# Kernel optimization log

Measured on AMD Instinct MI355X. Metric: run time of the kernel, lower is better.

The kernel has to match this reference:

```python
import jax, jax.numpy as jnp
import numpy as np
import math

L, B, T, S, D, H = 6, 4, 1024, 1024, 1024, 16
HD = D // H
SCALE = 1.0 / math.sqrt(HD)
EPS = 1e-5


def _ln(x, w, b):
    m = x.mean(-1, keepdims=True)
    v = ((x - m) ** 2).mean(-1, keepdims=True)
    return (x - m) * jax.lax.rsqrt(v + EPS) * w + b


def _mha(xq, xkv, qw, qb, kw, kb, vw, vb, ow, ob, mask):
    b, t, _ = xq.shape
    s = xkv.shape[1]
    q = (xq @ qw.T + qb).reshape(b, t, H, HD).transpose(0, 2, 1, 3)
    k = (xkv @ kw.T + kb).reshape(b, s, H, HD).transpose(0, 2, 1, 3)
    v = (xkv @ vw.T + vb).reshape(b, s, H, HD).transpose(0, 2, 1, 3)
    scores = jnp.einsum('bhqd,bhkd->bhqk', q, k) * SCALE
    scores = jnp.where(mask == 0, -jnp.inf, scores)
    attn = jax.nn.softmax(scores, axis=-1)  # dropout is identity (eval)
    o = jnp.einsum('bhqk,bhkd->bhqd', attn, v).transpose(0, 2, 1, 3).reshape(b, t, D)
    return o @ ow.T + ob


def _ffn(x, f1w, f1b, f2w, f2b, fnw, fnb):
    h = jax.nn.gelu(x @ f1w.T + f1b, approximate=False)
    y = h @ f2w.T + f2b
    return x + _ln(y, fnw, fnb)


def setup_inputs() -> dict:
    key = jax.random.key(0)
    ks = jax.random.split(key, 16)
    wf = lambda k: jax.random.normal(k, (L, D, D), jnp.float32) * 0.02
    zb = jnp.zeros((L, D), jnp.float32)
    ones = jnp.ones((L, D), jnp.float32)
    inp = {
        'x': jax.random.normal(ks[0], (B, T, D), jnp.float32),
        'enc_outputs': jax.random.normal(ks[1], (B, S, D), jnp.float32),
        'sqw': wf(ks[2]), 'sqb': zb, 'skw': wf(ks[3]), 'skb': zb,
        'svw': wf(ks[4]), 'svb': zb, 'sow': wf(ks[5]), 'sob': zb,
        'cqw': wf(ks[6]), 'cqb': zb, 'ckw': wf(ks[7]), 'ckb': zb,
        'cvw': wf(ks[8]), 'cvb': zb, 'cow': wf(ks[9]), 'cob': zb,
        'f1w': wf(ks[10]), 'f1b': zb, 'f2w': wf(ks[11]), 'f2b': zb,
        'fnw': ones, 'fnb': zb,
        'l1w': ones, 'l1b': zb, 'l2w': ones, 'l2b': zb, 'l3w': ones, 'l3b': zb,
        'src_mask': jnp.ones((1, 1, T, S), jnp.int32),
        'tgt_mask': jnp.tril(jnp.ones((T, T), jnp.int32))[None, None],
    }
    return inp


def reference(x, enc_outputs, sqw, sqb, skw, skb, svw, svb, sow, sob,
              cqw, cqb, ckw, ckb, cvw, cvb, cow, cob,
              f1w, f1b, f2w, f2b, fnw, fnb,
              l1w, l1b, l2w, l2b, l3w, l3b, src_mask, tgt_mask):
    for l in range(L):
        sa = _mha(x, x, sqw[l], sqb[l], skw[l], skb[l], svw[l], svb[l], sow[l], sob[l], tgt_mask)
        x = _ln(x + sa, l1w[l], l1b[l])
        ca = _mha(x, enc_outputs, cqw[l], cqb[l], ckw[l], ckb[l], cvw[l], cvb[l], cow[l], cob[l], src_mask)
        x = _ln(x + ca, l2w[l], l2b[l])
        ff = _ffn(x, f1w[l], f1b[l], f2w[l], f2b[l], fnw[l], fnb[l])
        x = _ln(x + ff, l3w[l], l3b[l])
    return x
```

## Files before the change

### kernel.cpp

```cpp
#include <hip/hip_runtime.h>
#include <stdint.h>

typedef unsigned short u16;
typedef unsigned int u32;
typedef __bf16 bf16x8 __attribute__((ext_vector_type(8)));
typedef float f32x4 __attribute__((ext_vector_type(4)));
typedef u16 u16x8 __attribute__((ext_vector_type(8)));
typedef u16 u16x4 __attribute__((ext_vector_type(4)));
typedef u32 u32x2 __attribute__((ext_vector_type(2)));

#define MFMA16(A, B, C) __builtin_amdgcn_mfma_f32_16x16x32_bf16((A), (B), (C), 0, 0, 0)

#define GLOAD_LDS16(GP, LP)                                                    \
  __builtin_amdgcn_global_load_lds(                                            \
      (__attribute__((address_space(1))) void*)(GP),                           \
      (__attribute__((address_space(3))) void*)(LP), 16, 0, 0)

__device__ __forceinline__ u16 f2bf(float f) {
  return __builtin_bit_cast(u16, (__bf16)f);
}

__device__ __forceinline__ float bf2f(u16 v) {
  return __builtin_bit_cast(float, ((u32)v) << 16);
}

__device__ __forceinline__ float exp2_raw(float x) {
  float r;
  asm("v_exp_f32 %0, %1\n\ts_nop 0" : "=v"(r) : "v"(x));
  return r;
}

__device__ __forceinline__ u32 cvt_pk_bf16(float lo, float hi) {
  u32 r;
  asm("v_cvt_pk_bf16_f32 %0, %1, %2" : "=v"(r) : "v"(lo), "v"(hi));
  return r;
}

#define SC2 0.1803368801111204f

struct WPtrs {
  const float* p[10];
};

__global__ __launch_bounds__(256) void wcvt_kernel(WPtrs w, u16* __restrict__ dst, int loff) {
  const int mat = blockIdx.y;
  const int i = blockIdx.x * 256 + threadIdx.x;
  float4 v = ((const float4*)(w.p[mat] + loff))[i];
  u16x4 o = {f2bf(v.x), f2bf(v.y), f2bf(v.z), f2bf(v.w)};
  ((u16x4*)dst)[(size_t)mat * gridDim.x * 256 + i] = o;
}

struct GemmArgs {
  const u16* A[3];
  const u16* W[3];
  const float* bias[3];
  u16* C[3];
  float scale[3];
};

__global__ __launch_bounds__(256, 4) void gemm_bt(GemmArgs g) {
  const int mat = blockIdx.y >> 3;
  const int n0 = (blockIdx.y & 7) * 128;
  const int m0 = blockIdx.x * 128;
  const int kz = blockIdx.z;
  const int kn = 16 / gridDim.z;
  const u16* __restrict__ A = g.A[mat];
  const u16* __restrict__ W = g.W[mat];

  __shared__ u16 As[128][64];
  __shared__ u16 Bs[128][64];

  const int tid = threadIdx.x;
  const int lane = tid & 63;
  const int wv = tid >> 6;
  const int wm = (wv >> 1) * 64;
  const int wn = (wv & 1) * 64;
  const int fr = lane & 15;
  const int fg = lane >> 4;

  f32x4 acc[4][4];
#pragma unroll
  for (int i = 0; i < 4; ++i)
#pragma unroll
    for (int j = 0; j < 4; ++j)
#pragma unroll
      for (int r = 0; r < 4; ++r) acc[i][j][r] = 0.f;

  const int row8 = lane >> 3;
  const int csw = ((lane & 7) ^ row8) * 8;
  const u16* ga = A + (size_t)(m0 + wv * 32 + row8) * 1024 + csw + kz * kn * 64;
  const u16* gb = W + (size_t)(n0 + wv * 32 + row8) * 1024 + csw + kz * kn * 64;

  for (int kt = 0; kt < kn; ++kt) {
    __syncthreads();
#pragma unroll
    for (int i = 0; i < 4; ++i) {
      GLOAD_LDS16(ga + (size_t)i * 8 * 1024, &As[wv * 32 + i * 8][0]);
      GLOAD_LDS16(gb + (size_t)i * 8 * 1024, &Bs[wv * 32 + i * 8][0]);
    }
    ga += 64;
    gb += 64;
    __syncthreads();
#pragma unroll
    for (int ks = 0; ks < 2; ++ks) {
      bf16x8 af[4], bfr[4];
#pragma unroll
      for (int i = 0; i < 4; ++i) {
        af[i] = *(const bf16x8*)&As[wm + i * 16 + fr][((ks * 4 + fg) ^ (fr & 7)) * 8];
        bfr[i] = *(const bf16x8*)&Bs[wn + i * 16 + fr][((ks * 4 + fg) ^ (fr & 7)) * 8];
      }
#pragma unroll
      for (int mi = 0; mi < 4; ++mi)
#pragma unroll
        for (int ni = 0; ni < 4; ++ni) acc[mi][ni] = MFMA16(af[mi], bfr[ni], acc[mi][ni]);
    }
  }

  const float* __restrict__ bias = g.bias[mat];
  const float scl = g.scale[mat];
  float bv[4];
#pragma unroll
  for (int ni = 0; ni < 4; ++ni) bv[ni] = (kz == 0) ? bias[n0 + wn + ni * 16 + fr] : 0.f;

  u16* __restrict__ C = g.C[mat] + (size_t)kz * (4096 * 1024);
#pragma unroll
  for (int mi = 0; mi < 4; ++mi) {
#pragma unroll
    for (int ni = 0; ni < 4; ++ni) {
      const int col = n0 + wn + ni * 16 + fr;
#pragma unroll
      for (int r = 0; r < 4; ++r) {
        const int row = m0 + wm + mi * 16 + fg * 4 + r;
        C[(size_t)row * 1024 + col] = f2bf((acc[mi][ni][r] + bv[ni]) * scl);
      }
    }
  }
}

template <int EPI>
__global__ __launch_bounds__(256, 4) void gemm_bt64(GemmArgs g) {
  const int n0 = blockIdx.y * 128;
  const int m0 = blockIdx.x * 64;
  const int kz = blockIdx.z;
  const int kn = 16 / gridDim.z;
  const u16* __restrict__ A = g.A[0];
  const u16* __restrict__ W = g.W[0];

  __shared__ u16 As[64][64];
  __shared__ u16 Bs[128][64];

  const int tid = threadIdx.x;
  const int lane = tid & 63;
  const int wv = tid >> 6;
  const int wm = (wv >> 1) * 32;
  const int wn = (wv & 1) * 64;
  const int fr = lane & 15;
  const int fg = lane >> 4;

  f32x4 acc[2][4];
#pragma unroll
  for (int i = 0; i < 2; ++i)
#pragma unroll
    for (int j = 0; j < 4; ++j)
#pragma unroll
      for (int r = 0; r < 4; ++r) acc[i][j][r] = 0.f;

  const int row8 = lane >> 3;
  const int csw = ((lane & 7) ^ row8) * 8;
  const u16* ga = A + (size_t)(m0 + wv * 16 + row8) * 1024 + csw + kz * kn * 64;
  const u16* gb = W + (size_t)(n0 + wv * 32 + row8) * 1024 + csw + kz * kn * 64;

  for (int kt = 0; kt < kn; ++kt) {
    __syncthreads();
    GLOAD_LDS16(ga, &As[wv * 16][0]);
    GLOAD_LDS16(ga + (size_t)8 * 1024, &As[wv * 16 + 8][0]);
#pragma unroll
    for (int i = 0; i < 4; ++i)
      GLOAD_LDS16(gb + (size_t)i * 8 * 1024, &Bs[wv * 32 + i * 8][0]);
    ga += 64;
    gb += 64;
    __syncthreads();
#pragma unroll
    for (int ks = 0; ks < 2; ++ks) {
      bf16x8 af[2], bfr[4];
#pragma unroll
      for (int i = 0; i < 2; ++i)
        af[i] = *(const bf16x8*)&As[wm + i * 16 + fr][((ks * 4 + fg) ^ (fr & 7)) * 8];
#pragma unroll
      for (int i = 0; i < 4; ++i)
        bfr[i] = *(const bf16x8*)&Bs[wn + i * 16 + fr][((ks * 4 + fg) ^ (fr & 7)) * 8];
#pragma unroll
      for (int mi = 0; mi < 2; ++mi)
#pragma unroll
        for (int ni = 0; ni < 4; ++ni) acc[mi][ni] = MFMA16(af[mi], bfr[ni], acc[mi][ni]);
    }
  }

  const float* __restrict__ bias = g.bias[0];
  float bv[4];
#pragma unroll
  for (int ni = 0; ni < 4; ++ni) bv[ni] = (kz == 0) ? bias[n0 + wn + ni * 16 + fr] : 0.f;

  u16* __restrict__ C = g.C[0] + (size_t)kz * (4096 * 1024);
#pragma unroll
  for (int mi = 0; mi < 2; ++mi) {
#pragma unroll
    for (int ni = 0; ni < 4; ++ni) {
      const int col = n0 + wn + ni * 16 + fr;
#pragma unroll
      for (int r = 0; r < 4; ++r) {
        const int row = m0 + wm + mi * 16 + fg * 4 + r;
        float v = acc[mi][ni][r] + bv[ni];
        if (EPI == 1) v = 0.5f * v * (1.0f + erff(v * 0.70710678118654752f));
        C[(size_t)row * 1024 + col] = f2bf(v);
      }
    }
  }
}

__global__ __launch_bounds__(512, 4) void attn_fwd(const u16* __restrict__ Q,
                                                   const u16* __restrict__ K,
                                                   const u16* __restrict__ V,
                                                   u16* __restrict__ O, int causal) {
  const int b = blockIdx.x >> 4;
  const int h = blockIdx.x & 15;
  const int qb = causal ? (7 - blockIdx.y) : blockIdx.y;
  const int tid = threadIdx.x;
  const int lane = tid & 63;
  const int wv = tid >> 6;
  const int fr = lane & 15;
  const int fg = lane >> 4;

  __shared__ u16 Ks[2][64][64];
  __shared__ u16 Vt[2][64][64];
  __shared__ u16 Plds[8][16][64];

  const int qrow0 = b * 1024 + qb * 128 + wv * 16;
  const int col0 = h * 64;

  const u16* qp = Q + (size_t)(qrow0 + fr) * 1024 + col0 + fg * 8;
  bf16x8 aQ0 = *(const bf16x8*)qp;
  bf16x8 aQ1 = *(const bf16x8*)(qp + 32);

  f32x4 ov[4];
#pragma unroll
  for (int i = 0; i < 4; ++i)
#pragma unroll
    for (int r = 0; r < 4; ++r) ov[i][r] = 0.f;
  float l_part = 0.f;

  const int kv_base = b * 1024;
  const int qg = qb * 128 + wv * 16 + fr;
  const int qg_max = qb * 128 + wv * 16 + 15;
  const int nt = causal ? (2 * qb + 2) : 16;

  const u16* gk0 = K + (size_t)(kv_base + wv * 16 + (lane >> 3)) * 1024 + col0 +
                   (((lane & 7) ^ (lane >> 3)) * 8);
  const int vt = tid - 256;
  const int kkp = vt & 31;
  const int d0 = (vt >> 5) * 8;
  const u16* gv0 = V + (size_t)(kv_base + 2 * kkp) * 1024 + col0 + d0;

#define STAGE_K(T, BUF)                                                        \
  if (wv < 4) {                                                                \
    const u16* gk = gk0 + (size_t)(T)*64 * 1024;                               \
    GLOAD_LDS16(gk, &Ks[BUF][wv * 16][0]);                                     \
    GLOAD_LDS16(gk + 8 * 1024, &Ks[BUF][wv * 16 + 8][0]);                      \
  }
#define LOAD_V(T)                                                              \
  if (tid >= 256) {                                                            \
    const u16* gvp = gv0 + (size_t)(T)*64 * 1024;                              \
    vr0 = *(const u16x8*)gvp;                                                  \
    vr1 = *(const u16x8*)(gvp + 1024);                                         \
  }
#define WRITE_V(BUF)                                                           \
  if (tid >= 256) {                                                            \
    _Pragma("unroll") for (int j = 0; j < 8; ++j) {                            \
      u32 pk = (u32)vr0[j] | ((u32)vr1[j] << 16);                              \
      *(u32*)&Vt[BUF][d0 + j][(((kkp >> 2) ^ j) * 8) + (kkp & 3) * 2] = pk;    \
    }                                                                          \
  }

  u16x8 vr0, vr1;
  STAGE_K(0, 0);
  LOAD_V(0);
  WRITE_V(0);

  for (int t = 0; t < nt; ++t) {
    const int cur = t & 1;
    __syncthreads();
    const bool pf = (t + 1 < nt);
    if (pf) {
      STAGE_K(t + 1, cur ^ 1);
      LOAD_V(t + 1);
    }

    const bool active = !causal || (t * 64 <= qg_max);
    if (active) {
      f32x4 st[4];
      __builtin_amdgcn_s_setprio(1);
#pragma unroll
      for (int hh = 0; hh < 4; ++hh) {
#pragma unroll
        for (int r = 0; r < 4; ++r) st[hh][r] = 0.f;
        const u16* krow = &Ks[cur][hh * 16 + fr][0];
        bf16x8 k0 = *(const bf16x8*)(krow + ((fg ^ (fr & 7)) * 8));
        bf16x8 k1 = *(const bf16x8*)(krow + (((4 + fg) ^ (fr & 7)) * 8));
        st[hh] = MFMA16(k0, aQ0, st[hh]);
        st[hh] = MFMA16(k1, aQ1, st[hh]);
      }
      __builtin_amdgcn_s_setprio(0);

      if (causal && t >= 2 * qb) {
#pragma unroll
        for (int hh = 0; hh < 4; ++hh)
#pragma unroll
          for (int r = 0; r < 4; ++r) {
            const int kkg = t * 64 + hh * 16 + fg * 4 + r;
            if (kkg > qg) st[hh][r] = -1e30f;
          }
      }

      float p[16];
#pragma unroll
      for (int hh = 0; hh < 4; ++hh)
#pragma unroll
        for (int r = 0; r < 4; ++r) {
          const float e = exp2_raw(st[hh][r]);
          p[hh * 4 + r] = e;
          l_part += e;
        }

#pragma unroll
      for (int hh = 0; hh < 4; ++hh) {
        u32x2 wpair = {cvt_pk_bf16(p[hh * 4 + 0], p[hh * 4 + 1]),
                       cvt_pk_bf16(p[hh * 4 + 2], p[hh * 4 + 3])};
        const int c = hh * 2 + (fg >> 1);
        *(u32x2*)&Plds[wv][fr][((c ^ (fr & 7)) * 8) + (fg & 1) * 4] = wpair;
      }
      bf16x8 pa[2];
#pragma unroll
      for (int ks = 0; ks < 2; ++ks)
        pa[ks] = *(const bf16x8*)&Plds[wv][fr][(((ks * 4 + fg) ^ (fr & 7)) * 8)];
      __builtin_amdgcn_s_setprio(1);
#pragma unroll
      for (int dt = 0; dt < 4; ++dt) {
#pragma unroll
        for (int ks = 0; ks < 2; ++ks) {
          bf16x8 bvv =
              *(const bf16x8*)&Vt[cur][dt * 16 + fr][(((ks * 4 + fg) ^ (fr & 7)) * 8)];
          ov[dt] = MFMA16(pa[ks], bvv, ov[dt]);
        }
      }
      __builtin_amdgcn_s_setprio(0);
    }

    if (pf) WRITE_V(cur ^ 1);
  }

  float ps = l_part;
  ps += __shfl_xor(ps, 16);
  ps += __shfl_xor(ps, 32);
  const float linv = 1.0f / ps;
  float fin[4];
#pragma unroll
  for (int r = 0; r < 4; ++r) fin[r] = __shfl(linv, fg * 4 + r);
#pragma unroll
  for (int dt = 0; dt < 4; ++dt)
#pragma unroll
    for (int r = 0; r < 4; ++r) {
      const int row = qrow0 + fg * 4 + r;
      const int col = col0 + dt * 16 + fr;
      O[(size_t)row * 1024 + col] = f2bf(ov[dt][r] * fin[r]);
    }
#undef STAGE_K
#undef LOAD_V
#undef WRITE_V
}

__device__ __forceinline__ float4 ld_bf4(const u16* p, size_t idx4) {
  u16x4 t = ((const u16x4*)p)[idx4];
  return make_float4(bf2f(t[0]), bf2f(t[1]), bf2f(t[2]), bf2f(t[3]));
}

__global__ __launch_bounds__(256) void ln_res_kernel(const u16* __restrict__ Xb_in,
                                                     const u16* __restrict__ T0,
                                                     const u16* __restrict__ T1, int nT,
                                                     const float* __restrict__ w,
                                                     const float* __restrict__ bia,
                                                     u16* __restrict__ Xb_out) {
  __shared__ float red[2][4];
  const int row = blockIdx.x;
  const int tid = threadIdx.x;
  const int lane = tid & 63, wv = tid >> 6;
  const size_t base4 = (size_t)row * 256;
  float4 xv = ld_bf4(Xb_in, base4 + tid);
  float4 tv = ld_bf4(T0, base4 + tid);
  float z0 = xv.x + tv.x, z1 = xv.y + tv.y, z2 = xv.z + tv.z, z3 = xv.w + tv.w;
  if (nT == 2) {
    float4 t1 = ld_bf4(T1, base4 + tid);
    z0 += t1.x; z1 += t1.y; z2 += t1.z; z3 += t1.w;
  }
  float s = z0 + z1 + z2 + z3;
  float ss = z0 * z0 + z1 * z1 + z2 * z2 + z3 * z3;
#pragma unroll
  for (int m = 1; m <= 32; m <<= 1) {
    s += __shfl_xor(s, m);
    ss += __shfl_xor(ss, m);
  }
  if (lane == 0) {
    red[0][wv] = s;
    red[1][wv] = ss;
  }
  __syncthreads();
  s = red[0][0] + red[0][1] + red[0][2] + red[0][3];
  ss = red[1][0] + red[1][1] + red[1][2] + red[1][3];
  const float mean = s * (1.f / 1024.f);
  const float var = ss * (1.f / 1024.f) - mean * mean;
  const float rs = rsqrtf(fmaxf(var, 0.f) + 1e-5f);
  float4 wv4 = ((const float4*)w)[tid];
  float4 bv4 = ((const float4*)bia)[tid];
  float o0 = (z0 - mean) * rs * wv4.x + bv4.x;
  float o1 = (z1 - mean) * rs * wv4.y + bv4.y;
  float o2 = (z2 - mean) * rs * wv4.z + bv4.z;
  float o3 = (z3 - mean) * rs * wv4.w + bv4.w;
  u16x4 ob = {f2bf(o0), f2bf(o1), f2bf(o2), f2bf(o3)};
  ((u16x4*)Xb_out)[base4 + tid] = ob;
}

__global__ __launch_bounds__(256) void ffn_ln_kernel(
    const u16* __restrict__ Xb, const u16* __restrict__ Y0, const u16* __restrict__ Y1,
    int nT, const float* __restrict__ fw_, const float* __restrict__ fb_,
    const float* __restrict__ w3, const float* __restrict__ b3, u16* __restrict__ Xb_out,
    float* __restrict__ Fout) {
  __shared__ float red[2][4];
  const int row = blockIdx.x;
  const int tid = threadIdx.x;
  const int lane = tid & 63, wv = tid >> 6;
  const size_t base4 = (size_t)row * 256;
  float4 yv = ld_bf4(Y0, base4 + tid);
  if (nT == 2) {
    float4 y1 = ld_bf4(Y1, base4 + tid);
    yv.x += y1.x; yv.y += y1.y; yv.z += y1.z; yv.w += y1.w;
  }
  float s = yv.x + yv.y + yv.z + yv.w;
  float ss = yv.x * yv.x + yv.y * yv.y + yv.z * yv.z + yv.w * yv.w;
#pragma unroll
  for (int m = 1; m <= 32; m <<= 1) {
    s += __shfl_xor(s, m);
    ss += __shfl_xor(ss, m);
  }
  if (lane == 0) {
    red[0][wv] = s;
    red[1][wv] = ss;
  }
  __syncthreads();
  s = red[0][0] + red[0][1] + red[0][2] + red[0][3];
  ss = red[1][0] + red[1][1] + red[1][2] + red[1][3];
  const float mean = s * (1.f / 1024.f);
  const float var = ss * (1.f / 1024.f) - mean * mean;
  const float rs = rsqrtf(fmaxf(var, 0.f) + 1e-5f);
  float4 xv = ld_bf4(Xb, base4 + tid);
  float4 fw4 = ((const float4*)fw_)[tid];
  float4 fb4 = ((const float4*)fb_)[tid];
  float z0 = 2.f * xv.x + (yv.x - mean) * rs * fw4.x + fb4.x;
  float z1 = 2.f * xv.y + (yv.y - mean) * rs * fw4.y + fb4.y;
  float z2 = 2.f * xv.z + (yv.z - mean) * rs * fw4.z + fb4.z;
  float z3 = 2.f * xv.w + (yv.w - mean) * rs * fw4.w + fb4.w;
  float s2 = z0 + z1 + z2 + z3;
  float ss2 = z0 * z0 + z1 * z1 + z2 * z2 + z3 * z3;
#pragma unroll
  for (int m = 1; m <= 32; m <<= 1) {
    s2 += __shfl_xor(s2, m);
    ss2 += __shfl_xor(ss2, m);
  }
  __syncthreads();
  if (lane == 0) {
    red[0][wv] = s2;
    red[1][wv] = ss2;
  }
  __syncthreads();
  s2 = red[0][0] + red[0][1] + red[0][2] + red[0][3];
  ss2 = red[1][0] + red[1][1] + red[1][2] + red[1][3];
  const float mean2 = s2 * (1.f / 1024.f);
  const float var2 = ss2 * (1.f / 1024.f) - mean2 * mean2;
  const float rs2 = rsqrtf(fmaxf(var2, 0.f) + 1e-5f);
  float4 w4 = ((const float4*)w3)[tid];
  float4 b4 = ((const float4*)b3)[tid];
  float o0 = (z0 - mean2) * rs2 * w4.x + b4.x;
  float o1 = (z1 - mean2) * rs2 * w4.y + b4.y;
  float o2 = (z2 - mean2) * rs2 * w4.z + b4.z;
  float o3 = (z3 - mean2) * rs2 * w4.w + b4.w;
  u16x4 ob = {f2bf(o0), f2bf(o1), f2bf(o2), f2bf(o3)};
  ((u16x4*)Xb_out)[base4 + tid] = ob;
  if (Fout) ((float4*)Fout)[base4 + tid] = make_float4(o0, o1, o2, o3);
}

__global__ __launch_bounds__(256) void cast2_kernel(const float* __restrict__ inA,
                                                    const float* __restrict__ inB,
                                                    u16* __restrict__ outA,
                                                    u16* __restrict__ outB) {
  const int bx = blockIdx.x;
  const float* in = (bx < 4096) ? inA : inB;
  u16* out = (bx < 4096) ? outA : outB;
  const size_t i = (size_t)(bx & 4095) * 256 + threadIdx.x;
  float4 v = ((const float4*)in)[i];
  u16x4 o = {f2bf(v.x), f2bf(v.y), f2bf(v.z), f2bf(v.w)};
  ((u16x4*)out)[i] = o;
}

extern "C" void kernel_launch(void* const* d_in, const int* in_sizes, int n_in, void* d_out,
                              int out_size, void* d_ws, size_t ws_size, hipStream_t stream) {
  const float* x_in = (const float*)d_in[0];
  const float* enc = (const float*)d_in[1];
  const float* sqw = (const float*)d_in[2];
  const float* sqb = (const float*)d_in[3];
  const float* skw = (const float*)d_in[4];
  const float* skb = (const float*)d_in[5];
  const float* svw = (const float*)d_in[6];
  const float* svb = (const float*)d_in[7];
  const float* sow = (const float*)d_in[8];
  const float* sob = (const float*)d_in[9];
  const float* cqw = (const float*)d_in[10];
  const float* cqb = (const float*)d_in[11];
  const float* ckw = (const float*)d_in[12];
  const float* ckb = (const float*)d_in[13];
  const float* cvw = (const float*)d_in[14];
  const float* cvb = (const float*)d_in[15];
  const float* cow = (const float*)d_in[16];
  const float* cob = (const float*)d_in[17];
  const float* f1w = (const float*)d_in[18];
  const float* f1b = (const float*)d_in[19];
  const float* f2w = (const float*)d_in[20];
  const float* f2b = (const float*)d_in[21];
  const float* fnw = (const float*)d_in[22];
  const float* fnb = (const float*)d_in[23];
  const float* l1w = (const float*)d_in[24];
  const float* l1b = (const float*)d_in[25];
  const float* l2w = (const float*)d_in[26];
  const float* l2b = (const float*)d_in[27];
  const float* l3w = (const float*)d_in[28];
  const float* l3b = (const float*)d_in[29];

  const size_t MB = 1024 * 1024;
  const int ALLW = (ws_size >= 200 * MB) ? 1 : 0;
  const int NS = (ws_size >= 90 * MB) ? 2 : 1;
  char* ws = (char*)d_ws;
  u16* tmpb = (u16*)ws;
  char* p = ws + (size_t)NS * 8 * MB;
  u16* xb = (u16*)p;   p += 8 * MB;
  u16* encb = (u16*)p; p += 8 * MB;
  u16* qbuf = (u16*)p; p += 8 * MB;
  u16* kbuf = (u16*)p; p += 8 * MB;
  u16* vbuf = (u16*)p; p += 8 * MB;
  u16* wbf = (u16*)p;
  u16* tmpb1 = tmpb + (size_t)4 * 1024 * 1024;
  const size_t W1M = 1024 * 1024;

  cast2_kernel<<<8192, 256, 0, stream>>>(x_in, enc, xb, encb);

  WPtrs wp;
  wp.p[0] = sqw; wp.p[1] = skw; wp.p[2] = svw; wp.p[3] = sow;
  wp.p[4] = cqw; wp.p[5] = ckw; wp.p[6] = cvw; wp.p[7] = cow;
  wp.p[8] = f1w; wp.p[9] = f2w;

  if (ALLW) wcvt_kernel<<<dim3(6144, 10), 256, 0, stream>>>(wp, wbf, 0);

  for (int l = 0; l < 6; ++l) {
    const size_t bo = (size_t)l * 1024;
    if (!ALLW) wcvt_kernel<<<dim3(1024, 10), 256, 0, stream>>>(wp, wbf, l * (int)W1M);
    #define WT(t) (ALLW ? (wbf + ((size_t)(t)*6 + l) * W1M) : (wbf + (size_t)(t)*W1M))

    GemmArgs g;
    g.scale[0] = SC2; g.scale[1] = 1.f; g.scale[2] = 1.f;
    g.A[0] = xb; g.A[1] = xb; g.A[2] = xb;
    g.W[0] = WT(0); g.W[1] = WT(1); g.W[2] = WT(2);
    g.bias[0] = sqb + bo; g.bias[1] = skb + bo; g.bias[2] = svb + bo;
    g.C[0] = qbuf; g.C[1] = kbuf; g.C[2] = vbuf;
    gemm_bt<<<dim3(32, 24, 1), 256, 0, stream>>>(g);
    attn_fwd<<<dim3(64, 8), 512, 0, stream>>>(qbuf, kbuf, vbuf, qbuf, 1);
    g.scale[0] = 1.f;
    g.A[0] = qbuf; g.W[0] = WT(3); g.bias[0] = sob + bo; g.C[0] = tmpb;
    gemm_bt64<0><<<dim3(64, 8, NS), 256, 0, stream>>>(g);
    ln_res_kernel<<<4096, 256, 0, stream>>>(xb, tmpb, tmpb1, NS, l1w + bo, l1b + bo, xb);

    g.scale[0] = SC2;
    g.A[0] = xb; g.A[1] = encb; g.A[2] = encb;
    g.W[0] = WT(4); g.W[1] = WT(5); g.W[2] = WT(6);
    g.bias[0] = cqb + bo; g.bias[1] = ckb + bo; g.bias[2] = cvb + bo;
    g.C[0] = qbuf; g.C[1] = kbuf; g.C[2] = vbuf;
    gemm_bt<<<dim3(32, 24, 1), 256, 0, stream>>>(g);
    attn_fwd<<<dim3(64, 8), 512, 0, stream>>>(qbuf, kbuf, vbuf, qbuf, 0);
    g.scale[0] = 1.f;
    g.A[0] = qbuf; g.W[0] = WT(7); g.bias[0] = cob + bo; g.C[0] = tmpb;
    gemm_bt64<0><<<dim3(64, 8, NS), 256, 0, stream>>>(g);
    ln_res_kernel<<<4096, 256, 0, stream>>>(xb, tmpb, tmpb1, NS, l2w + bo, l2b + bo, xb);

    g.A[0] = xb; g.W[0] = WT(8); g.bias[0] = f1b + bo; g.C[0] = kbuf;
    gemm_bt64<1><<<dim3(64, 8, 1), 256, 0, stream>>>(g);
    g.A[0] = kbuf; g.W[0] = WT(9); g.bias[0] = f2b + bo; g.C[0] = tmpb;
    gemm_bt64<0><<<dim3(64, 8, NS), 256, 0, stream>>>(g);
    float* fo = (l == 5) ? (float*)d_out : nullptr;
    ffn_ln_kernel<<<4096, 256, 0, stream>>>(xb, tmpb, tmpb1, NS, fnw + bo, fnb + bo, l3w + bo,
                                            l3b + bo, xb, fo);
    #undef WT
  }
}
```

Before: 1.311 ms.

## Split attention KV range across two blocks and merge partial outputs

Attention gains a template variant that splits each (batch, head, query-block) KV loop into two halves, indexed by blockIdx.z. Each half writes an unnormalised bf16 partial output plus per-row softmax denominators, and a new merge kernel sums the two partials and normalises. The aim is to double the number of attention blocks for better CU occupancy and to even out the load imbalance of causal blocks. In exchange it adds an extra kernel launch and extra memory traffic per attention call. The split path is only enabled when the workspace is large, and the all-weights threshold moves slightly to make room for the denominator buffer.

```diff
diff --git a/kernel.cpp b/kernel.cpp
--- a/kernel.cpp
+++ b/kernel.cpp
@@ -218,10 +218,12 @@
   }
 }
 
+template <int SPLIT>
 __global__ __launch_bounds__(512, 4) void attn_fwd(const u16* __restrict__ Q,
                                                    const u16* __restrict__ K,
                                                    const u16* __restrict__ V,
-                                                   u16* __restrict__ O, int causal) {
+                                                   u16* __restrict__ O,
+                                                   float* __restrict__ lb, int causal) {
   const int b = blockIdx.x >> 4;
   const int h = blockIdx.x & 15;
   const int qb = causal ? (7 - blockIdx.y) : blockIdx.y;
@@ -253,6 +255,12 @@
   const int qg = qb * 128 + wv * 16 + fr;
   const int qg_max = qb * 128 + wv * 16 + 15;
   const int nt = causal ? (2 * qb + 2) : 16;
+  int tbeg = 0, tend = nt;
+  if (SPLIT) {
+    const int h0 = nt >> 1;
+    tbeg = blockIdx.z ? h0 : 0;
+    tend = blockIdx.z ? nt : h0;
+  }
 
   const u16* gk0 = K + (size_t)(kv_base + wv * 16 + (lane >> 3)) * 1024 + col0 +
                    (((lane & 7) ^ (lane >> 3)) * 8);
@@ -282,14 +290,14 @@
   }
 
   u16x8 vr0, vr1;
-  STAGE_K(0, 0);
-  LOAD_V(0);
+  STAGE_K(tbeg, 0);
+  LOAD_V(tbeg);
   WRITE_V(0);
 
-  for (int t = 0; t < nt; ++t) {
-    const int cur = t & 1;
+  for (int t = tbeg; t < tend; ++t) {
+    const int cur = (t - tbeg) & 1;
     __syncthreads();
-    const bool pf = (t + 1 < nt);
+    const bool pf = (t + 1 < tend);
     if (pf) {
       STAGE_K(t + 1, cur ^ 1);
       LOAD_V(t + 1);
@@ -361,18 +369,34 @@
   float ps = l_part;
   ps += __shfl_xor(ps, 16);
   ps += __shfl_xor(ps, 32);
-  const float linv = 1.0f / ps;
-  float fin[4];
-#pragma unroll
-  for (int r = 0; r < 4; ++r) fin[r] = __shfl(linv, fg * 4 + r);
-#pragma unroll
-  for (int dt = 0; dt < 4; ++dt)
-#pragma unroll
-    for (int r = 0; r < 4; ++r) {
-      const int row = qrow0 + fg * 4 + r;
-      const int col = col0 + dt * 16 + fr;
-      O[(size_t)row * 1024 + col] = f2bf(ov[dt][r] * fin[r]);
-    }
+
+  if (SPLIT) {
+    u16* __restrict__ Os = O + (size_t)blockIdx.z * (4096 * 1024);
+#pragma unroll
+    for (int dt = 0; dt < 4; ++dt)
+#pragma unroll
+      for (int r = 0; r < 4; ++r) {
+        const int row = qrow0 + fg * 4 + r;
+        const int col = col0 + dt * 16 + fr;
+        Os[(size_t)row * 1024 + col] = f2bf(ov[dt][r]);
+      }
+    if (lane < 16 && wv == (tid >> 6))
+      lb[(size_t)blockIdx.z * 65536 + (size_t)(b * 16 + h) * 1024 + qb * 128 + wv * 16 +
+         lane] = ps;
+  } else {
+    const float linv = 1.0f / ps;
+    float fin[4];
+#pragma unroll
+    for (int r = 0; r < 4; ++r) fin[r] = __shfl(linv, fg * 4 + r);
+#pragma unroll
+    for (int dt = 0; dt < 4; ++dt)
+#pragma unroll
+      for (int r = 0; r < 4; ++r) {
+        const int row = qrow0 + fg * 4 + r;
+        const int col = col0 + dt * 16 + fr;
+        O[(size_t)row * 1024 + col] = f2bf(ov[dt][r] * fin[r]);
+      }
+  }
 #undef STAGE_K
 #undef LOAD_V
 #undef WRITE_V
@@ -381,6 +405,23 @@
 __device__ __forceinline__ float4 ld_bf4(const u16* p, size_t idx4) {
   u16x4 t = ((const u16x4*)p)[idx4];
   return make_float4(bf2f(t[0]), bf2f(t[1]), bf2f(t[2]), bf2f(t[3]));
+}
+
+__global__ __launch_bounds__(256) void attn_merge(const u16* __restrict__ O0,
+                                                  const float* __restrict__ lb,
+                                                  u16* __restrict__ Oout) {
+  const int r = blockIdx.x;
+  const int tid = threadIdx.x;
+  const int b = r >> 10, t = r & 1023;
+  const int h = tid >> 4;
+  const size_t li = (size_t)(b * 16 + h) * 1024 + t;
+  const float inv = 1.0f / (lb[li] + lb[65536 + li]);
+  const size_t i4 = (size_t)r * 256 + tid;
+  float4 a = ld_bf4(O0, i4);
+  float4 c = ld_bf4(O0 + (size_t)4096 * 1024, i4);
+  u16x4 o = {f2bf((a.x + c.x) * inv), f2bf((a.y + c.y) * inv), f2bf((a.z + c.z) * inv),
+             f2bf((a.w + c.w) * inv)};
+  ((u16x4*)Oout)[i4] = o;
 }
 
 __global__ __launch_bounds__(256) void ln_res_kernel(const u16* __restrict__ Xb_in,
@@ -543,8 +584,9 @@
   const float* l3b = (const float*)d_in[29];
 
   const size_t MB = 1024 * 1024;
-  const int ALLW = (ws_size >= 200 * MB) ? 1 : 0;
+  const int ALLW = (ws_size >= 201 * MB) ? 1 : 0;
   const int NS = (ws_size >= 90 * MB) ? 2 : 1;
+  const int SPL = (ALLW && NS == 2) ? 1 : 0;
   char* ws = (char*)d_ws;
   u16* tmpb = (u16*)ws;
   char* p = ws + (size_t)NS * 8 * MB;
@@ -553,7 +595,8 @@
   u16* qbuf = (u16*)p; p += 8 * MB;
   u16* kbuf = (u16*)p; p += 8 * MB;
   u16* vbuf = (u16*)p; p += 8 * MB;
-  u16* wbf = (u16*)p;
+  u16* wbf = (u16*)p;  p += (ALLW ? 120 : 20) * MB;
+  float* lbuf = (float*)p;
   u16* tmpb1 = tmpb + (size_t)4 * 1024 * 1024;
   const size_t W1M = 1024 * 1024;
 
@@ -570,6 +613,15 @@
     const size_t bo = (size_t)l * 1024;
     if (!ALLW) wcvt_kernel<<<dim3(1024, 10), 256, 0, stream>>>(wp, wbf, l * (int)W1M);
     #define WT(t) (ALLW ? (wbf + ((size_t)(t)*6 + l) * W1M) : (wbf + (size_t)(t)*W1M))
+    #define RUN_ATTN(CAUSAL)                                                          \
+      if (SPL) {                                                                      \
+        attn_fwd<1><<<dim3(64, 8, 2), 512, 0, stream>>>(qbuf, kbuf, vbuf, tmpb, lbuf, \
+                                                        (CAUSAL));                    \
+        attn_merge<<<4096, 256, 0, stream>>>(tmpb, lbuf, qbuf);                       \
+      } else {                                                                        \
+        attn_fwd<0><<<dim3(64, 8, 1), 512, 0, stream>>>(qbuf, kbuf, vbuf, qbuf, lbuf, \
+                                                        (CAUSAL));                    \
+      }
 
     GemmArgs g;
     g.scale[0] = SC2; g.scale[1] = 1.f; g.scale[2] = 1.f;
@@ -578,7 +630,7 @@
     g.bias[0] = sqb + bo; g.bias[1] = skb + bo; g.bias[2] = svb + bo;
     g.C[0] = qbuf; g.C[1] = kbuf; g.C[2] = vbuf;
     gemm_bt<<<dim3(32, 24, 1), 256, 0, stream>>>(g);
-    attn_fwd<<<dim3(64, 8), 512, 0, stream>>>(qbuf, kbuf, vbuf, qbuf, 1);
+    RUN_ATTN(1);
     g.scale[0] = 1.f;
     g.A[0] = qbuf; g.W[0] = WT(3); g.bias[0] = sob + bo; g.C[0] = tmpb;
     gemm_bt64<0><<<dim3(64, 8, NS), 256, 0, stream>>>(g);
@@ -590,7 +642,7 @@
     g.bias[0] = cqb + bo; g.bias[1] = ckb + bo; g.bias[2] = cvb + bo;
     g.C[0] = qbuf; g.C[1] = kbuf; g.C[2] = vbuf;
     gemm_bt<<<dim3(32, 24, 1), 256, 0, stream>>>(g);
-    attn_fwd<<<dim3(64, 8), 512, 0, stream>>>(qbuf, kbuf, vbuf, qbuf, 0);
+    RUN_ATTN(0);
     g.scale[0] = 1.f;
     g.A[0] = qbuf; g.W[0] = WT(7); g.bias[0] = cob + bo; g.C[0] = tmpb;
     gemm_bt64<0><<<dim3(64, 8, NS), 256, 0, stream>>>(g);
@@ -604,5 +656,6 @@
     ffn_ln_kernel<<<4096, 256, 0, stream>>>(xb, tmpb, tmpb1, NS, fnw + bo, fnb + bo, l3w + bo,
                                             l3b + bo, xb, fo);
     #undef WT
-  }
-}
+    #undef RUN_ATTN
+  }
+}
```

Measured after the change: 1.389 ms. +5.9%, slower.
